# Optimization experiments

Measured on AMD Instinct MI355X. Metric: run time of the kernel, lower is better.

Reference implementation:

```python
import jax, jax.numpy as jnp
import numpy as np


def setup_inputs() -> dict:
    key = jax.random.key(0)
    kx, ky = jax.random.split(key)
    B, SX, SY, D = 8, 2048, 2048, 512
    x = jax.random.normal(kx, (B, SX, D), dtype=jnp.float32)
    y = jax.random.normal(ky, (B, SY, D), dtype=jnp.float32)
    return {"x": x, "y": y}


def reference(x, y):
    # e = x @ y^T : [B, Sx, Sy]
    e = jnp.einsum("bsd,btd->bst", x, y)
    ai = jax.nn.softmax(e, axis=-1)
    # a = ai @ y : [B, Sx, D]
    a = jnp.einsum("bst,btd->bsd", ai, y)
    # concat [x, a] along feature dim -> [B, Sx, 2D]; dropout in eval mode = identity
    out = jnp.concatenate([x, a], axis=-1)
    return out
```

## Files before the change

### kernel.cpp

```cpp
#include <hip/hip_runtime.h>
#include <stdint.h>

typedef _Float16 half4v __attribute__((ext_vector_type(4)));
typedef _Float16 half8v __attribute__((ext_vector_type(8)));
typedef float    f32x4  __attribute__((ext_vector_type(4)));
typedef __attribute__((address_space(3))) void       lds_void;
typedef const __attribute__((address_space(1))) void g_void;

#define NB 8
#define SXX 2048
#define DD 512
#define QBLK 64
#define TBLK 64
#define NITER 32

#define RSB 1040u
#define BUFSZ (64u * RSB)
#define POFF  (2u * BUFSZ)
#define PR    136u
#define SCOFF (POFF + 64u * PR)
#define LIOFF (SCOFF + 256u)
#define LDS_BYTES 142336
#define YH_BYTES (8ull * 2048ull * 512ull * 2ull)

__global__ __launch_bounds__(256)
void convert_y(const float* __restrict__ y, _Float16* __restrict__ yh) {
  const int i = (blockIdx.x * 256 + threadIdx.x) * 8;
  f32x4 f0 = *(const f32x4*)(y + i);
  f32x4 f1 = *(const f32x4*)(y + i + 4);
  half8v h;
  h[0]=(_Float16)f0[0]; h[1]=(_Float16)f0[1]; h[2]=(_Float16)f0[2]; h[3]=(_Float16)f0[3];
  h[4]=(_Float16)f1[0]; h[5]=(_Float16)f1[1]; h[6]=(_Float16)f1[2]; h[7]=(_Float16)f1[3];
  *(half8v*)(yh + i) = h;
}

template <bool USE_WS>
__global__ __launch_bounds__(512, 2)
void attn_fused(const float* __restrict__ x, const float* __restrict__ y,
                const _Float16* __restrict__ yh, float* __restrict__ out) {
  extern __shared__ char smem[];
  const int bid   = blockIdx.x;
  const int b     = bid & 7;
  const int qtile = bid >> 3;
  const int tid   = threadIdx.x;
  const int w     = tid >> 6;
  const int lane  = tid & 63;
  const int l15   = lane & 15;
  const int g     = lane >> 4;

  const float*    xb  = x + (size_t)b * SXX * DD;
  const float*    yb  = y + (size_t)b * SXX * DD;
  const _Float16* yhb = USE_WS ? (yh + (size_t)b * SXX * DD) : nullptr;
  float* outb = out + (size_t)b * SXX * (2 * DD);
  const int qbase = qtile * QBLK;

  if (USE_WS) {
#pragma unroll
    for (int i = 0; i < 8; ++i) {
      const int row = w * 8 + i;
      __builtin_amdgcn_global_load_lds((g_void*)(yhb + row * DD + lane * 8),
                                       (lds_void*)(smem + (uint32_t)row * RSB), 16, 0, 0);
    }
  }

  {
    const f32x4* src = (const f32x4*)(xb + (size_t)qbase * DD);
    for (int i = tid; i < QBLK * (DD / 4); i += 512) {
      f32x4 v = src[i];
      *(f32x4*)(outb + (size_t)(qbase + (i >> 7)) * (2 * DD) + (i & 127) * 4) = v;
    }
  }

  half8v bq[16];
  if (w < 4) {
    const float* xr = xb + (size_t)(qbase + w * 16 + l15) * DD;
#pragma unroll
    for (int c = 0; c < 16; ++c) {
      const int d0 = c * 32 + g * 8;
      f32x4 f0 = *(const f32x4*)(xr + d0);
      f32x4 f1 = *(const f32x4*)(xr + d0 + 4);
      half8v h;
      h[0] = (_Float16)f0[0]; h[1] = (_Float16)f0[1];
      h[2] = (_Float16)f0[2]; h[3] = (_Float16)f0[3];
      h[4] = (_Float16)f1[0]; h[5] = (_Float16)f1[1];
      h[6] = (_Float16)f1[2]; h[7] = (_Float16)f1[3];
      bq[c] = h;
    }
  }

  if (!USE_WS) {
#pragma unroll
    for (int k = 0; k < 8; ++k) {
      const int u = tid + k * 512;
      const int t = u >> 6, c8 = u & 63;
      const float* p = yb + t * DD + c8 * 8;
      f32x4 f0 = *(const f32x4*)p, f1 = *(const f32x4*)(p + 4);
      half8v h;
      h[0]=(_Float16)f0[0]; h[1]=(_Float16)f0[1]; h[2]=(_Float16)f0[2]; h[3]=(_Float16)f0[3];
      h[4]=(_Float16)f1[0]; h[5]=(_Float16)f1[1]; h[6]=(_Float16)f1[2]; h[7]=(_Float16)f1[3];
      *(half8v*)(smem + (uint32_t)t * RSB + (uint32_t)c8 * 16u) = h;
    }
  }

  f32x4 acc[4][4];
#pragma unroll
  for (int i = 0; i < 4; ++i)
#pragma unroll
    for (int j = 0; j < 4; ++j) acc[i][j] = (f32x4){0.f, 0.f, 0.f, 0.f};
  float mrun = -3.0e38f, lrun = 0.0f;

  __syncthreads();

  for (int it = 0; it < NITER; ++it) {
    const uint32_t cb  = (uint32_t)(it & 1) * BUFSZ;
    const uint32_t nb2 = cb ^ BUFSZ;

    if (USE_WS && it + 1 < NITER) {
      const _Float16* src = yhb + (size_t)(it + 1) * TBLK * DD;
#pragma unroll
      for (int i = 0; i < 8; ++i) {
        const int row = w * 8 + i;
        __builtin_amdgcn_global_load_lds((g_void*)(src + row * DD + lane * 8),
                                         (lds_void*)(smem + nb2 + (uint32_t)row * RSB), 16, 0, 0);
      }
    }

    if (w < 4) {
      f32x4 st[4];
#pragma unroll
      for (int tt = 0; tt < 4; ++tt) st[tt] = (f32x4){0.f, 0.f, 0.f, 0.f};
#pragma unroll
      for (int c = 0; c < 16; ++c) {
        const uint32_t db = cb + 64u * (uint32_t)c + 16u * (uint32_t)g;
#pragma unroll
        for (int tt = 0; tt < 4; ++tt) {
          const half8v af = *(const half8v*)(smem + (uint32_t)(tt * 16 + l15) * RSB + db);
          st[tt] = __builtin_amdgcn_mfma_f32_16x16x32_f16(af, bq[c], st[tt], 0, 0, 0);
        }
      }

      float tmax = -3.0e38f;
#pragma unroll
      for (int tt = 0; tt < 4; ++tt)
#pragma unroll
        for (int r = 0; r < 4; ++r) tmax = fmaxf(tmax, st[tt][r]);
      tmax = fmaxf(tmax, __shfl_xor(tmax, 16));
      tmax = fmaxf(tmax, __shfl_xor(tmax, 32));
      const float mnew = fmaxf(mrun, tmax);
      float pvv[16];
      float rsum = 0.f;
#pragma unroll
      for (int tt = 0; tt < 4; ++tt)
#pragma unroll
        for (int r = 0; r < 4; ++r) {
          const float e = __expf(st[tt][r] - mnew);
          pvv[tt * 4 + r] = e;
          rsum += e;
        }
      rsum += __shfl_xor(rsum, 16);
      rsum += __shfl_xor(rsum, 32);
      const float scale = __expf(mrun - mnew);
      lrun = lrun * scale + rsum;
      mrun = mnew;

#pragma unroll
      for (int tt = 0; tt < 4; ++tt) {
        half4v hv;
        hv[0] = (_Float16)pvv[tt * 4 + 0]; hv[1] = (_Float16)pvv[tt * 4 + 1];
        hv[2] = (_Float16)pvv[tt * 4 + 2]; hv[3] = (_Float16)pvv[tt * 4 + 3];
        *(half4v*)(smem + POFF + (uint32_t)(w * 16 + l15) * PR +
                   (uint32_t)tt * 32u + (uint32_t)g * 8u) = hv;
      }
      if (g == 0) ((float*)(smem + SCOFF))[w * 16 + l15] = scale;
    }

    if (!USE_WS && it + 1 < NITER) {
      const float* ybt = yb + (size_t)(it + 1) * TBLK * DD;
#pragma unroll
      for (int k = 0; k < 8; ++k) {
        const int u = tid + k * 512;
        const int t = u >> 6, c8 = u & 63;
        const float* p = ybt + t * DD + c8 * 8;
        f32x4 f0 = *(const f32x4*)p, f1 = *(const f32x4*)(p + 4);
        half8v h;
        h[0]=(_Float16)f0[0]; h[1]=(_Float16)f0[1]; h[2]=(_Float16)f0[2]; h[3]=(_Float16)f0[3];
        h[4]=(_Float16)f1[0]; h[5]=(_Float16)f1[1]; h[6]=(_Float16)f1[2]; h[7]=(_Float16)f1[3];
        *(half8v*)(smem + nb2 + (uint32_t)t * RSB + (uint32_t)c8 * 16u) = h;
      }
    }

    __syncthreads();

    {
#pragma unroll
      for (int qq = 0; qq < 4; ++qq) {
        const f32x4 s4 = *(const f32x4*)(smem + SCOFF + (uint32_t)(qq * 16 + 4 * g) * 4u);
#pragma unroll
        for (int dtl = 0; dtl < 4; ++dtl) {
          acc[qq][dtl][0] *= s4[0]; acc[qq][dtl][1] *= s4[1];
          acc[qq][dtl][2] *= s4[2]; acc[qq][dtl][3] *= s4[3];
        }
      }
      __builtin_amdgcn_sched_barrier(0);

      half4v palo[4][2], pahi[4][2];
      const uint32_t pb = POFF + (uint32_t)l15 * PR + (uint32_t)g * 8u;
#pragma unroll
      for (int qq = 0; qq < 4; ++qq)
#pragma unroll
        for (int ch = 0; ch < 2; ++ch) {
          const uint32_t a = pb + (uint32_t)qq * (16u * PR) + (uint32_t)ch * 64u;
          asm volatile("ds_read_b64 %0, %1" : "=v"(palo[qq][ch]) : "v"(a));
          asm volatile("ds_read_b64 %0, %1" : "=v"(pahi[qq][ch]) : "v"(a + 32u));
        }
      half4v blo[8], bhi[8];
      const uint32_t tb = cb + (uint32_t)(4 * g + (l15 >> 2)) * RSB +
                          (uint32_t)(l15 & 3) * 8u + (uint32_t)w * 128u;
#pragma unroll
      for (int fr = 0; fr < 8; ++fr) {
        const uint32_t a = tb + (uint32_t)(fr >> 2) * (32u * RSB) + (uint32_t)(fr & 3) * 32u;
        asm volatile("ds_read_b64_tr_b16 %0, %1" : "=v"(blo[fr]) : "v"(a));
        asm volatile("ds_read_b64_tr_b16 %0, %1" : "=v"(bhi[fr]) : "v"(a + 16u * RSB));
      }
      asm volatile("s_waitcnt lgkmcnt(0)" ::: "memory");
      __builtin_amdgcn_sched_barrier(0);

#pragma unroll
      for (int fr = 0; fr < 8; ++fr) {
        const half8v b8 = __builtin_shufflevector(blo[fr], bhi[fr], 0, 1, 2, 3, 4, 5, 6, 7);
        const int ch = fr >> 2, dtl = fr & 3;
#pragma unroll
        for (int qq = 0; qq < 4; ++qq) {
          const half8v pa = __builtin_shufflevector(palo[qq][ch], pahi[qq][ch],
                                                    0, 1, 2, 3, 4, 5, 6, 7);
          acc[qq][dtl] = __builtin_amdgcn_mfma_f32_16x16x32_f16(pa, b8, acc[qq][dtl], 0, 0, 0);
        }
      }
    }
    __syncthreads();
  }

  if (w < 4 && g == 0) ((float*)(smem + LIOFF))[w * 16 + l15] = 1.0f / lrun;
  __syncthreads();
#pragma unroll
  for (int qq = 0; qq < 4; ++qq) {
    const f32x4 iv = *(const f32x4*)(smem + LIOFF + (uint32_t)(qq * 16 + 4 * g) * 4u);
#pragma unroll
    for (int dtl = 0; dtl < 4; ++dtl) {
#pragma unroll
      for (int r = 0; r < 4; ++r) {
        const int q = qbase + qq * 16 + 4 * g + r;
        outb[(size_t)q * (2 * DD) + DD + w * 64 + dtl * 16 + l15] = acc[qq][dtl][r] * iv[r];
      }
    }
  }
}

extern "C" void kernel_launch(void* const* d_in, const int* in_sizes, int n_in,
                              void* d_out, int out_size, void* d_ws, size_t ws_size,
                              hipStream_t stream) {
  (void)in_sizes; (void)n_in; (void)out_size;
  const float* x = (const float*)d_in[0];
  const float* y = (const float*)d_in[1];
  float* out = (float*)d_out;
  static_assert(LDS_BYTES <= 160 * 1024, "LDS over budget");
  const bool use_ws = (ws_size >= YH_BYTES);
  if (use_ws) {
    _Float16* yh = (_Float16*)d_ws;
    hipLaunchKernelGGL(convert_y, dim3(4096), dim3(256), 0, stream, y, yh);
    hipFuncSetAttribute((const void*)attn_fused<true>,
                        hipFuncAttributeMaxDynamicSharedMemorySize, LDS_BYTES);
    hipLaunchKernelGGL((attn_fused<true>), dim3((SXX / QBLK) * NB), dim3(512),
                       LDS_BYTES, stream, x, y, yh, out);
  } else {
    hipFuncSetAttribute((const void*)attn_fused<false>,
                        hipFuncAttributeMaxDynamicSharedMemorySize, LDS_BYTES);
    hipLaunchKernelGGL((attn_fused<false>), dim3((SXX / QBLK) * NB), dim3(512),
                       LDS_BYTES, stream, x, y, nullptr, out);
  }
}
```

Measured before the change: 116.3 us.

## Split QK^T and softmax across all eight waves with cross-wave max exchange

Before, only four of the eight waves computed the score tile and the online softmax, so the other half sat idle during that phase. Now every wave computes half of the key columns (32 of 64) for its 16 query rows. The row max is exchanged through shared memory with an extra block barrier, and partial row sums are kept per half and combined at the end. This balances the MFMA and exp work across the waves, at the cost of one extra __syncthreads per iteration and a bit more LDS.

```diff
diff --git a/kernel.cpp b/kernel.cpp
--- a/kernel.cpp
+++ b/kernel.cpp
@@ -19,8 +19,9 @@
 #define POFF  (2u * BUFSZ)
 #define PR    136u
 #define SCOFF (POFF + 64u * PR)
-#define LIOFF (SCOFF + 256u)
-#define LDS_BYTES 142336
+#define TMOFF (SCOFF + 256u)
+#define LOFF  (TMOFF + 512u)
+#define LDS_BYTES 143104
 #define YH_BYTES (8ull * 2048ull * 512ull * 2ull)
 
 __global__ __launch_bounds__(256)
@@ -47,6 +48,8 @@
   const int lane  = tid & 63;
   const int l15   = lane & 15;
   const int g     = lane >> 4;
+  const int qw    = w & 3;
+  const int th    = w >> 2;
 
   const float*    xb  = x + (size_t)b * SXX * DD;
   const float*    yb  = y + (size_t)b * SXX * DD;
@@ -72,8 +75,8 @@
   }
 
   half8v bq[16];
-  if (w < 4) {
-    const float* xr = xb + (size_t)(qbase + w * 16 + l15) * DD;
+  {
+    const float* xr = xb + (size_t)(qbase + qw * 16 + l15) * DD;
 #pragma unroll
     for (int c = 0; c < 16; ++c) {
       const int d0 = c * 32 + g * 8;
@@ -125,54 +128,58 @@
       }
     }
 
-    if (w < 4) {
-      f32x4 st[4];
-#pragma unroll
-      for (int tt = 0; tt < 4; ++tt) st[tt] = (f32x4){0.f, 0.f, 0.f, 0.f};
-#pragma unroll
-      for (int c = 0; c < 16; ++c) {
-        const uint32_t db = cb + 64u * (uint32_t)c + 16u * (uint32_t)g;
-#pragma unroll
-        for (int tt = 0; tt < 4; ++tt) {
-          const half8v af = *(const half8v*)(smem + (uint32_t)(tt * 16 + l15) * RSB + db);
-          st[tt] = __builtin_amdgcn_mfma_f32_16x16x32_f16(af, bq[c], st[tt], 0, 0, 0);
-        }
-      }
-
-      float tmax = -3.0e38f;
-#pragma unroll
-      for (int tt = 0; tt < 4; ++tt)
-#pragma unroll
-        for (int r = 0; r < 4; ++r) tmax = fmaxf(tmax, st[tt][r]);
-      tmax = fmaxf(tmax, __shfl_xor(tmax, 16));
-      tmax = fmaxf(tmax, __shfl_xor(tmax, 32));
-      const float mnew = fmaxf(mrun, tmax);
-      float pvv[16];
-      float rsum = 0.f;
-#pragma unroll
-      for (int tt = 0; tt < 4; ++tt)
-#pragma unroll
-        for (int r = 0; r < 4; ++r) {
-          const float e = __expf(st[tt][r] - mnew);
-          pvv[tt * 4 + r] = e;
-          rsum += e;
-        }
-      rsum += __shfl_xor(rsum, 16);
-      rsum += __shfl_xor(rsum, 32);
-      const float scale = __expf(mrun - mnew);
-      lrun = lrun * scale + rsum;
-      mrun = mnew;
-
-#pragma unroll
-      for (int tt = 0; tt < 4; ++tt) {
-        half4v hv;
-        hv[0] = (_Float16)pvv[tt * 4 + 0]; hv[1] = (_Float16)pvv[tt * 4 + 1];
-        hv[2] = (_Float16)pvv[tt * 4 + 2]; hv[3] = (_Float16)pvv[tt * 4 + 3];
-        *(half4v*)(smem + POFF + (uint32_t)(w * 16 + l15) * PR +
-                   (uint32_t)tt * 32u + (uint32_t)g * 8u) = hv;
-      }
-      if (g == 0) ((float*)(smem + SCOFF))[w * 16 + l15] = scale;
-    }
+    f32x4 st[2];
+    st[0] = (f32x4){0.f, 0.f, 0.f, 0.f};
+    st[1] = (f32x4){0.f, 0.f, 0.f, 0.f};
+#pragma unroll
+    for (int c = 0; c < 16; ++c) {
+      const uint32_t db = cb + 64u * (uint32_t)c + 16u * (uint32_t)g;
+#pragma unroll
+      for (int tt = 0; tt < 2; ++tt) {
+        const half8v af =
+            *(const half8v*)(smem + (uint32_t)(th * 32 + tt * 16 + l15) * RSB + db);
+        st[tt] = __builtin_amdgcn_mfma_f32_16x16x32_f16(af, bq[c], st[tt], 0, 0, 0);
+      }
+    }
+
+    float tmax = -3.0e38f;
+#pragma unroll
+    for (int tt = 0; tt < 2; ++tt)
+#pragma unroll
+      for (int r = 0; r < 4; ++r) tmax = fmaxf(tmax, st[tt][r]);
+    tmax = fmaxf(tmax, __shfl_xor(tmax, 16));
+    tmax = fmaxf(tmax, __shfl_xor(tmax, 32));
+    if (g == 0) ((float*)(smem + TMOFF))[th * 64 + qw * 16 + l15] = tmax;
+    __syncthreads();
+    const float tm0 = ((float*)(smem + TMOFF))[qw * 16 + l15];
+    const float tm1 = ((float*)(smem + TMOFF))[64 + qw * 16 + l15];
+    const float mnew = fmaxf(mrun, fmaxf(tm0, tm1));
+
+    float pvv[8];
+    float rsum = 0.f;
+#pragma unroll
+    for (int tt = 0; tt < 2; ++tt)
+#pragma unroll
+      for (int r = 0; r < 4; ++r) {
+        const float e = __expf(st[tt][r] - mnew);
+        pvv[tt * 4 + r] = e;
+        rsum += e;
+      }
+    rsum += __shfl_xor(rsum, 16);
+    rsum += __shfl_xor(rsum, 32);
+    const float scale = __expf(mrun - mnew);
+    lrun = lrun * scale + rsum;
+    mrun = mnew;
+
+#pragma unroll
+    for (int tt = 0; tt < 2; ++tt) {
+      half4v hv;
+      hv[0] = (_Float16)pvv[tt * 4 + 0]; hv[1] = (_Float16)pvv[tt * 4 + 1];
+      hv[2] = (_Float16)pvv[tt * 4 + 2]; hv[3] = (_Float16)pvv[tt * 4 + 3];
+      *(half4v*)(smem + POFF + (uint32_t)(qw * 16 + l15) * PR +
+                 (uint32_t)(th * 64 + tt * 32) + (uint32_t)g * 8u) = hv;
+    }
+    if (th == 0 && g == 0) ((float*)(smem + SCOFF))[qw * 16 + l15] = scale;
 
     if (!USE_WS && it + 1 < NITER) {
       const float* ybt = yb + (size_t)(it + 1) * TBLK * DD;
@@ -240,11 +247,15 @@
     __syncthreads();
   }
 
-  if (w < 4 && g == 0) ((float*)(smem + LIOFF))[w * 16 + l15] = 1.0f / lrun;
+  if (g == 0) ((float*)(smem + LOFF))[th * 64 + qw * 16 + l15] = lrun;
   __syncthreads();
 #pragma unroll
   for (int qq = 0; qq < 4; ++qq) {
-    const f32x4 iv = *(const f32x4*)(smem + LIOFF + (uint32_t)(qq * 16 + 4 * g) * 4u);
+    const f32x4 l0 = *(const f32x4*)(smem + LOFF + (uint32_t)(qq * 16 + 4 * g) * 4u);
+    const f32x4 l1 = *(const f32x4*)(smem + LOFF + 256u + (uint32_t)(qq * 16 + 4 * g) * 4u);
+    f32x4 iv;
+#pragma unroll
+    for (int r = 0; r < 4; ++r) iv[r] = 1.0f / (l0[r] + l1[r]);
 #pragma unroll
     for (int dtl = 0; dtl < 4; ++dtl) {
 #pragma unroll
```

New measurement: 115.6 us. No clear change (-0.7%).
